# Performance work log

Hardware: AMD Instinct MI355X
Metric: run time of the kernel (lower is better)

Reference implementation:

```python
import jax, jax.numpy as jnp
import numpy as np

N = 100000   # nodes
E = 1600000  # edges
F_IN = 64    # n_features
H = 32       # hidden_size
OUT = 1      # output_size


def _lin(k, fan_in, fan_out):
    return (jax.random.normal(k, (fan_in, fan_out), jnp.float32) / np.sqrt(fan_in)).astype(jnp.float32)


def setup_inputs() -> dict:
    key = jax.random.key(0)
    ks = jax.random.split(key, 16)
    x = jax.random.normal(ks[0], (N, F_IN), jnp.float32)
    edge_index = jax.random.randint(ks[1], (2, E), 0, N, dtype=jnp.int64)
    # guarantee current_node (=0) has outgoing edges so the legal-move mask is non-empty
    edge_index = edge_index.at[0, :64].set(0)
    edge_attr = jax.random.uniform(ks[2], (E,), jnp.float32)
    return {
        "x": x, "edge_index": edge_index, "edge_attr": edge_attr, "current_node": 0,
        # conv_in: GraphConv(F_IN -> H)
        "Win_rel": _lin(ks[3], F_IN, H), "bin_rel": jnp.zeros((H,), jnp.float32), "Win_root": _lin(ks[4], F_IN, H),
        # conv_hidden: GraphConv(H -> H)
        "Wh_rel": _lin(ks[5], H, H), "bh_rel": jnp.zeros((H,), jnp.float32), "Wh_root": _lin(ks[6], H, H),
        # policy_conv: GraphConv(H -> OUT)
        "Wp_rel": _lin(ks[7], H, OUT), "bp_rel": jnp.zeros((OUT,), jnp.float32), "Wp_root": _lin(ks[8], H, OUT),
        # value_conv: GraphConv(H -> OUT)
        "Wv_rel": _lin(ks[9], H, OUT), "bv_rel": jnp.zeros((OUT,), jnp.float32), "Wv_root": _lin(ks[10], H, OUT),
    }


def _graph_conv(h, src, dst, ew, W_rel, b_rel, W_root):
    # PyG GraphConv: out_i = W_root h_i + W_rel * sum_{j->i} e_ji * h_j + b
    msg = h[src] * ew[:, None]                              # [E, d] gather + scale
    agg = jax.ops.segment_sum(msg, dst, num_segments=N)      # [N, d] scatter-add
    return agg @ W_rel + b_rel + h @ W_root


def reference(x, edge_index, edge_attr, current_node,
              Win_rel, bin_rel, Win_root,
              Wh_rel, bh_rel, Wh_root,
              Wp_rel, bp_rel, Wp_root,
              Wv_rel, bv_rel, Wv_root):
    src, dst = edge_index[0], edge_index[1]
    h = jax.nn.relu(_graph_conv(x, src, dst, edge_attr, Win_rel, bin_rel, Win_root))
    h = jax.nn.relu(_graph_conv(h, src, dst, edge_attr, Wh_rel, bh_rel, Wh_root))
    p = _graph_conv(h, src, dst, edge_attr, Wp_rel, bp_rel, Wp_root)  # [N, 1]
    v = _graph_conv(h, src, dst, edge_attr, Wv_rel, bv_rel, Wv_root)  # [N, 1]
    # illegal_moves_mask: 1 for nodes directly reachable from current_node
    hit = (src == current_node).astype(jnp.float32)
    mask = (jnp.zeros((N,), jnp.float32).at[dst].add(hit) > 0).astype(jnp.float32)
    p_m = mask * p.T                                   # [1, N]
    p_m = jnp.where(p_m == 0, -jnp.inf, p_m)
    p_soft = jax.nn.softmax(p_m, axis=1)
    v_m = mask * v.T                                   # [1, N]
    return p_soft.reshape(-1), v_m.reshape(-1)
```

## Files before the change

kernel.cpp:

```cpp
#include <hip/hip_runtime.h>
#include <hip/hip_fp16.h>
#include <cmath>

static constexpr int NN = 100000;
static constexpr int NE = 1600000;
static const size_t NW = (size_t)NN * 32;
static constexpr int SUB = 256;
static constexpr int NSUB = 391;
static constexpr int CH = 8192;
static constexpr int NCH = (NE + CH - 1) / CH;
static constexpr int BCAP = 5200;
static constexpr int CSRN = NSUB * BCAP;
static constexpr int MCAP = 4096;
static constexpr int NCAP = 8192;

__device__ __forceinline__ float ent_w(unsigned e)
{
    return __half2float(__ushort_as_half((unsigned short)(e >> 17)));
}
__device__ __forceinline__ int ent_s(unsigned e)
{
    int s = (int)(e & 0x1FFFF);
    return s < NN ? s : NN - 1;
}

__device__ __forceinline__ float4 pack8(const float* v)
{
    union { __half2 h2[4]; float4 f4; } u;
    u.h2[0] = __floats2half2_rn(v[0], v[1]);
    u.h2[1] = __floats2half2_rn(v[2], v[3]);
    u.h2[2] = __floats2half2_rn(v[4], v[5]);
    u.h2[3] = __floats2half2_rn(v[6], v[7]);
    return u.f4;
}

__device__ __forceinline__ int wave_incl_scan(int v, int lane)
{
    int s = v;
#pragma unroll
    for (int d = 1; d < 64; d <<= 1) {
        int o = __shfl_up(s, d, 64);
        if (lane >= d) s += o;
    }
    return s;
}

__global__ void __launch_bounds__(512) fused_build_mm1_k(
    const int* __restrict__ src, const int* __restrict__ dst,
    const float* __restrict__ ew, const int* __restrict__ curp,
    int* __restrict__ maskb, int* __restrict__ mcount, int* __restrict__ mlist,
    int* __restrict__ bcnt, unsigned* __restrict__ bx,
    unsigned char* __restrict__ bd,
    const float* __restrict__ x, const float* __restrict__ Wrel,
    const float* __restrict__ Wroot, const float* __restrict__ bin,
    __half* __restrict__ proj1, __half* __restrict__ root1)
{
    __shared__ union {
        struct {
            unsigned sBufX[CH];
            unsigned char sBufD[CH];
            int lhist[NSUB];
            int lpos[NSUB];
            int lstart[NSUB];
            int lbase[NSUB];
            int tscan[512];
        } s;
        struct {
            float sX[128 * 65];
            float sW[64 * 68];
        } m;
    } u;

    int t = threadIdx.x;
    int bid = blockIdx.x;

    if (bid < NCH) {
        for (int i = t; i < NSUB; i += 512) { u.s.lhist[i] = 0; u.s.lpos[i] = 0; }
        __syncthreads();
        int c0 = bid * CH;
        int cur = curp[0];
        unsigned rx[CH / 512];
        int rd[CH / 512];
#pragma unroll
        for (int it = 0; it < CH / 512; ++it) {
            int e = c0 + it * 512 + t;
            rd[it] = -1;
            if (e < NE) {
                int d = dst[e];
                int sv = src[e];
                if ((unsigned)d < (unsigned)NN) {
                    rd[it] = d;
                    unsigned bits = __half_as_ushort(__float2half(ew[e]));
                    rx[it] = ((unsigned)sv & 0x1FFFF) | (bits << 17);
                    atomicAdd(&u.s.lhist[d >> 8], 1);
                    if (sv == cur) {
                        if (atomicExch(maskb + d, 1) == 0) {
                            int idx = atomicAdd(mcount, 1);
                            if (idx < MCAP) mlist[idx] = d;
                        }
                    }
                }
            }
        }
        __syncthreads();
        {
            int v = (t < NSUB) ? u.s.lhist[t] : 0;
            int lane = t & 63, wv = t >> 6;
            int sI = wave_incl_scan(v, lane);
            if (lane == 63) u.s.tscan[wv] = sI;
            __syncthreads();
            if (t == 0) {
                int r = 0;
#pragma unroll
                for (int w2 = 0; w2 < 8; ++w2) {
                    int xw = u.s.tscan[w2];
                    u.s.tscan[8 + w2] = r;
                    r += xw;
                }
            }
            __syncthreads();
            if (t < NSUB) {
                u.s.lstart[t] = sI + u.s.tscan[8 + wv] - v;
                u.s.lbase[t] = (v > 0) ? atomicAdd(&bcnt[t], v) : 0;
            }
        }
        __syncthreads();
#pragma unroll
        for (int it = 0; it < CH / 512; ++it) {
            if (rd[it] >= 0) {
                int b = rd[it] >> 8;
                int p = atomicAdd(&u.s.lpos[b], 1);
                int pos = u.s.lstart[b] + p;
                u.s.sBufX[pos] = rx[it];
                u.s.sBufD[pos] = (unsigned char)(rd[it] & 255);
            }
        }
        __syncthreads();
        int grp = t >> 4, l16 = t & 15;
        for (int b = grp; b < NSUB; b += 32) {
            int s0 = u.s.lstart[b];
            int cb = u.s.lhist[b];
            int gb = u.s.lbase[b];
            size_t gb0 = (size_t)b * BCAP;
            for (int j = l16; j < cb; j += 16) {
                unsigned pos = (unsigned)(gb + j);
                if (pos < (unsigned)BCAP) {
                    bx[gb0 + pos] = u.s.sBufX[s0 + j];
                    bd[gb0 + pos] = u.s.sBufD[s0 + j];
                }
            }
        }
    } else {
        int mb = bid - NCH;
        for (int i = t; i < 64 * 32; i += 512) {
            int k = i >> 5, j = i & 31;
            u.m.sW[k * 68 + j] = Wrel[i];
            u.m.sW[k * 68 + 32 + j] = Wroot[i];
        }
        int base = mb * 128;
        for (int i = t; i < 2048; i += 512) {
            int node = i >> 4;
            int k = (i & 15) * 4;
            int n = base + node;
            if (n >= NN) n = NN - 1;
            float4 v4 = *(const float4*)(x + (size_t)n * 64 + k);
            float* p = u.m.sX + node * 65 + k;
            p[0] = v4.x; p[1] = v4.y; p[2] = v4.z; p[3] = v4.w;
        }
        __syncthreads();
        int cg = t & 7;
        int ng = t >> 3;
        int c0m = 8 * cg;
        float acc[2][8] = {};
        for (int k = 0; k < 64; ++k) {
            float xv0 = u.m.sX[(2 * ng + 0) * 65 + k];
            float xv1 = u.m.sX[(2 * ng + 1) * 65 + k];
            float4 w0 = *(const float4*)(u.m.sW + k * 68 + c0m);
            float4 w1 = *(const float4*)(u.m.sW + k * 68 + c0m + 4);
            const float* wp = (const float*)&w0;
#pragma unroll
            for (int j = 0; j < 4; ++j) {
                float w = wp[j];
                acc[0][j] = fmaf(xv0, w, acc[0][j]);
                acc[1][j] = fmaf(xv1, w, acc[1][j]);
            }
            const float* wq = (const float*)&w1;
#pragma unroll
            for (int j = 0; j < 4; ++j) {
                float w = wq[j];
                acc[0][4 + j] = fmaf(xv0, w, acc[0][4 + j]);
                acc[1][4 + j] = fmaf(xv1, w, acc[1][4 + j]);
            }
        }
#pragma unroll
        for (int r = 0; r < 2; ++r) {
            int n = base + 2 * ng + r;
            if (n >= NN) break;
            if (cg < 4) {
                *(float4*)(proj1 + (size_t)n * 32 + c0m) = pack8(acc[r]);
            } else {
                int c = c0m - 32;
                float vv[8];
#pragma unroll
                for (int j = 0; j < 8; ++j) vv[j] = acc[r][j] + bin[c + j];
                *(float4*)(root1 + (size_t)n * 32 + c) = pack8(vv);
            }
        }
    }
}

__global__ void __launch_bounds__(1024) sortagg1_k(
    const unsigned* __restrict__ bx, const unsigned char* __restrict__ bd,
    const int* __restrict__ bcnt, const int* __restrict__ maskb,
    int* __restrict__ needb, int* __restrict__ ncount,
    int* __restrict__ needlist,
    const __half* __restrict__ proj1, const __half* __restrict__ root1,
    unsigned* __restrict__ csr4, int* __restrict__ deg, int* __restrict__ off,
    __half* __restrict__ h1)
{
    __shared__ unsigned sX[BCAP];
    __shared__ unsigned char sD[BCAP];
    __shared__ unsigned sE[BCAP];
    __shared__ int lhist[SUB];
    __shared__ int lstart[SUB];
    __shared__ int lcur[SUB];
    __shared__ int tscan[16];
    int g = blockIdx.x, t = threadIdx.x;
    if (t < SUB) { lhist[t] = 0; lcur[t] = 0; }
    __syncthreads();
    int cnt = bcnt[g];
    if (cnt < 0) cnt = 0;
    if (cnt > BCAP) cnt = BCAP;
    size_t gbase = (size_t)g * BCAP;
    for (int i = t; i < cnt; i += 1024) {
        unsigned e = bx[gbase + i];
        unsigned char d = bd[gbase + i];
        sX[i] = e;
        sD[i] = d;
        atomicAdd(&lhist[d], 1);
    }
    __syncthreads();
    {
        int v = (t < SUB) ? lhist[t] : 0;
        int lane = t & 63, wv = t >> 6;
        int sI = wave_incl_scan(v, lane);
        if (t < SUB && lane == 63) tscan[wv] = sI;
        __syncthreads();
        if (t == 0) {
            int r = 0;
#pragma unroll
            for (int w2 = 0; w2 < 4; ++w2) {
                int xw = tscan[w2];
                tscan[8 + w2] = r;
                r += xw;
            }
        }
        __syncthreads();
        if (t < SUB) lstart[t] = sI + tscan[8 + wv] - v;
    }
    __syncthreads();
    for (int i = t; i < cnt; i += 1024) {
        int ld = (int)sD[i];
        int p = atomicAdd(&lcur[ld], 1);
        int pos = lstart[ld] + p;
        if ((unsigned)pos < (unsigned)BCAP) sE[pos] = sX[i];
    }
    __syncthreads();
    int base = g * BCAP;
    if (t < SUB) {
        int n = g * SUB + t;
        if (n < NN) {
            deg[n] = lhist[t];
            off[n] = base + lstart[t];
            if (maskb[n] != 0) {
                if (atomicExch(needb + n, 1) == 0) {
                    int ix = atomicAdd(ncount, 1);
                    if (ix < NCAP) needlist[ix] = n;
                }
                int s0 = lstart[t], dgn = lhist[t];
                for (int i2 = 0; i2 < dgn; ++i2) {
                    int s = ent_s(sE[s0 + i2]);
                    if (atomicExch(needb + s, 1) == 0) {
                        int ix = atomicAdd(ncount, 1);
                        if (ix < NCAP) needlist[ix] = s;
                    }
                }
            }
        }
    }
    for (int i = t; i < cnt; i += 1024) {
        unsigned pos = (unsigned)(base + i);
        if (pos < (unsigned)CSRN) csr4[pos] = sE[i];
    }
    int q = t & 3;
    int f0 = q * 8;
    int l = t >> 2;
    int n = g * SUB + l;
    if (n >= NN) return;
    int st = lstart[l];
    int dg = lhist[l];
    if (st < 0) st = 0;
    if (st > BCAP) st = BCAP;
    if (dg < 0) dg = 0;
    if (dg > BCAP - st) dg = BCAP - st;
    float acc[8] = {0.f, 0.f, 0.f, 0.f, 0.f, 0.f, 0.f, 0.f};
    int i = 0;
    for (; i + 1 < dg; i += 2) {
        unsigned e0 = sE[st + i];
        unsigned e1 = sE[st + i + 1];
        float w0 = ent_w(e0), w1 = ent_w(e1);
        float4 r0 = *(const float4*)(proj1 + (size_t)ent_s(e0) * 32 + f0);
        float4 r1 = *(const float4*)(proj1 + (size_t)ent_s(e1) * 32 + f0);
        const __half2* h0 = (const __half2*)&r0;
        const __half2* h1p = (const __half2*)&r1;
#pragma unroll
        for (int u = 0; u < 4; ++u) {
            float2 a = __half22float2(h0[u]);
            float2 b = __half22float2(h1p[u]);
            acc[2 * u] = fmaf(w0, a.x, acc[2 * u]);
            acc[2 * u + 1] = fmaf(w0, a.y, acc[2 * u + 1]);
            acc[2 * u] = fmaf(w1, b.x, acc[2 * u]);
            acc[2 * u + 1] = fmaf(w1, b.y, acc[2 * u + 1]);
        }
    }
    if (i < dg) {
        unsigned e0 = sE[st + i];
        float w0 = ent_w(e0);
        float4 r0 = *(const float4*)(proj1 + (size_t)ent_s(e0) * 32 + f0);
        const __half2* h0 = (const __half2*)&r0;
#pragma unroll
        for (int u = 0; u < 4; ++u) {
            float2 a = __half22float2(h0[u]);
            acc[2 * u] = fmaf(w0, a.x, acc[2 * u]);
            acc[2 * u + 1] = fmaf(w0, a.y, acc[2 * u + 1]);
        }
    }
    float4 rr = *(const float4*)(root1 + (size_t)n * 32 + f0);
    const __half2* rp = (const __half2*)&rr;
    float h[8];
#pragma unroll
    for (int u = 0; u < 4; ++u) {
        float2 f2 = __half22float2(rp[u]);
        h[2 * u] = fmaxf(acc[2 * u] + f2.x, 0.f);
        h[2 * u + 1] = fmaxf(acc[2 * u + 1] + f2.y, 0.f);
    }
    *(float4*)(h1 + (size_t)n * 32 + f0) = pack8(h);
}

__global__ void __launch_bounds__(256) mm2_k(
    const __half* __restrict__ h1, const float* __restrict__ Wrel,
    const float* __restrict__ Wroot, const float* __restrict__ bh,
    __half* __restrict__ proj2, __half* __restrict__ root2)
{
    __shared__ float sX[128 * 33];
    __shared__ float sW[32 * 68];
    int t = threadIdx.x;
    for (int i = t; i < 32 * 32; i += 256) {
        int k = i >> 5, j = i & 31;
        sW[k * 68 + j] = Wrel[i];
        sW[k * 68 + 32 + j] = Wroot[i];
    }
    int base = blockIdx.x * 128;
    for (int i = t; i < 512; i += 256) {
        int node = i >> 2;
        int hs = (i & 3) * 8;
        int n = base + node;
        if (n >= NN) n = NN - 1;
        float4 v = *(const float4*)(h1 + (size_t)n * 32 + hs);
        const __half2* hp = (const __half2*)&v;
        float* p = sX + node * 33 + hs;
#pragma unroll
        for (int u = 0; u < 4; ++u) {
            float2 f2 = __half22float2(hp[u]);
            p[2 * u] = f2.x;
            p[2 * u + 1] = f2.y;
        }
    }
    __syncthreads();
    int cg = t & 7;
    int ng = t >> 3;
    int c0 = 8 * cg;
    float acc[4][8] = {};
    for (int k = 0; k < 32; ++k) {
        float xv0 = sX[(4 * ng + 0) * 33 + k];
        float xv1 = sX[(4 * ng + 1) * 33 + k];
        float xv2 = sX[(4 * ng + 2) * 33 + k];
        float xv3 = sX[(4 * ng + 3) * 33 + k];
        float4 w0 = *(const float4*)(sW + k * 68 + c0);
        float4 w1 = *(const float4*)(sW + k * 68 + c0 + 4);
        const float* wp = (const float*)&w0;
#pragma unroll
        for (int j = 0; j < 4; ++j) {
            float w = wp[j];
            acc[0][j] = fmaf(xv0, w, acc[0][j]);
            acc[1][j] = fmaf(xv1, w, acc[1][j]);
            acc[2][j] = fmaf(xv2, w, acc[2][j]);
            acc[3][j] = fmaf(xv3, w, acc[3][j]);
        }
        const float* wq = (const float*)&w1;
#pragma unroll
        for (int j = 0; j < 4; ++j) {
            float w = wq[j];
            acc[0][4 + j] = fmaf(xv0, w, acc[0][4 + j]);
            acc[1][4 + j] = fmaf(xv1, w, acc[1][4 + j]);
            acc[2][4 + j] = fmaf(xv2, w, acc[2][4 + j]);
            acc[3][4 + j] = fmaf(xv3, w, acc[3][4 + j]);
        }
    }
#pragma unroll
    for (int r = 0; r < 4; ++r) {
        int n = base + 4 * ng + r;
        if (n >= NN) break;
        if (cg < 4) {
            *(float4*)(proj2 + (size_t)n * 32 + c0) = pack8(acc[r]);
        } else {
            int c = c0 - 32;
            float v[8];
#pragma unroll
            for (int j = 0; j < 8; ++j) v[j] = acc[r][j] + bh[c + j];
            *(float4*)(root2 + (size_t)n * 32 + c) = pack8(v);
        }
    }
}

__global__ void __launch_bounds__(256) need_gather_k(
    const __half* __restrict__ proj2, const __half* __restrict__ root2,
    const float* __restrict__ Wp_rel, const float* __restrict__ Wp_root,
    const float* __restrict__ bp, const float* __restrict__ Wv_rel,
    const float* __restrict__ Wv_root, const float* __restrict__ bv,
    const unsigned* __restrict__ csr4, const int* __restrict__ off,
    const int* __restrict__ deg, const int* __restrict__ needlist,
    const int* __restrict__ ncount, float2* __restrict__ pv,
    float* __restrict__ pbase, float* __restrict__ vbase)
{
    __shared__ float sHead[4 * 32];
    if (threadIdx.x < 32) {
        sHead[threadIdx.x] = Wp_rel[threadIdx.x];
        sHead[32 + threadIdx.x] = Wp_root[threadIdx.x];
        sHead[64 + threadIdx.x] = Wv_rel[threadIdx.x];
        sHead[96 + threadIdx.x] = Wv_root[threadIdx.x];
    }
    __syncthreads();
    int t = threadIdx.x;
    int q = t & 3;
    int f0 = q * 8;
    int m = ncount[0];
    if (m > NCAP) m = NCAP;
    int idx = blockIdx.x * 64 + (t >> 2);
    if (idx >= m) return;
    int n = needlist[idx];
    if ((unsigned)n >= (unsigned)NN) n = 0;
    int st = off[n];
    int dg = deg[n];
    if (st < 0) st = 0;
    if (st > CSRN) st = CSRN;
    if (dg < 0) dg = 0;
    if (dg > CSRN - st) dg = CSRN - st;
    float acc[8] = {0.f, 0.f, 0.f, 0.f, 0.f, 0.f, 0.f, 0.f};
    int i = 0;
    for (; i + 3 < dg; i += 4) {
        unsigned e0 = csr4[st + i];
        unsigned e1 = csr4[st + i + 1];
        unsigned e2 = csr4[st + i + 2];
        unsigned e3 = csr4[st + i + 3];
        float4 r0 = *(const float4*)(proj2 + (size_t)ent_s(e0) * 32 + f0);
        float4 r1 = *(const float4*)(proj2 + (size_t)ent_s(e1) * 32 + f0);
        float4 r2 = *(const float4*)(proj2 + (size_t)ent_s(e2) * 32 + f0);
        float4 r3 = *(const float4*)(proj2 + (size_t)ent_s(e3) * 32 + f0);
        float w0 = ent_w(e0), w1 = ent_w(e1), w2 = ent_w(e2), w3 = ent_w(e3);
        const __half2* h0 = (const __half2*)&r0;
        const __half2* h1p = (const __half2*)&r1;
        const __half2* h2p = (const __half2*)&r2;
        const __half2* h3p = (const __half2*)&r3;
#pragma unroll
        for (int u = 0; u < 4; ++u) {
            float2 a = __half22float2(h0[u]);
            float2 b = __half22float2(h1p[u]);
            float2 c = __half22float2(h2p[u]);
            float2 d = __half22float2(h3p[u]);
            acc[2 * u]     = fmaf(w0, a.x, acc[2 * u]);
            acc[2 * u + 1] = fmaf(w0, a.y, acc[2 * u + 1]);
            acc[2 * u]     = fmaf(w1, b.x, acc[2 * u]);
            acc[2 * u + 1] = fmaf(w1, b.y, acc[2 * u + 1]);
            acc[2 * u]     = fmaf(w2, c.x, acc[2 * u]);
            acc[2 * u + 1] = fmaf(w2, c.y, acc[2 * u + 1]);
            acc[2 * u]     = fmaf(w3, d.x, acc[2 * u]);
            acc[2 * u + 1] = fmaf(w3, d.y, acc[2 * u + 1]);
        }
    }
    for (; i < dg; ++i) {
        unsigned e0 = csr4[st + i];
        float w0 = ent_w(e0);
        float4 r0 = *(const float4*)(proj2 + (size_t)ent_s(e0) * 32 + f0);
        const __half2* h0 = (const __half2*)&r0;
#pragma unroll
        for (int u = 0; u < 4; ++u) {
            float2 a = __half22float2(h0[u]);
            acc[2 * u] = fmaf(w0, a.x, acc[2 * u]);
            acc[2 * u + 1] = fmaf(w0, a.y, acc[2 * u + 1]);
        }
    }
    float4 rr = *(const float4*)(root2 + (size_t)n * 32 + f0);
    const __half2* rp = (const __half2*)&rr;
    float h[8];
#pragma unroll
    for (int u = 0; u < 4; ++u) {
        float2 f2 = __half22float2(rp[u]);
        h[2 * u] = fmaxf(acc[2 * u] + f2.x, 0.f);
        h[2 * u + 1] = fmaxf(acc[2 * u + 1] + f2.y, 0.f);
    }
    float prv = 0.f, pov = 0.f, vrv = 0.f, vov = 0.f;
#pragma unroll
    for (int j = 0; j < 8; ++j) {
        prv = fmaf(h[j], sHead[f0 + j], prv);
        pov = fmaf(h[j], sHead[32 + f0 + j], pov);
        vrv = fmaf(h[j], sHead[64 + f0 + j], vrv);
        vov = fmaf(h[j], sHead[96 + f0 + j], vov);
    }
#pragma unroll
    for (int mm = 1; mm <= 2; mm <<= 1) {
        prv += __shfl_xor(prv, mm, 64);
        pov += __shfl_xor(pov, mm, 64);
        vrv += __shfl_xor(vrv, mm, 64);
        vov += __shfl_xor(vov, mm, 64);
    }
    if (q == 0) {
        pv[n] = make_float2(prv, vrv);
        pbase[n] = pov + bp[0];
        vbase[n] = vov + bv[0];
    }
}

__global__ void __launch_bounds__(256) masked_softmax_k(
    const int* __restrict__ mlist, const int* __restrict__ mcount,
    const unsigned* __restrict__ csr4, const int* __restrict__ off,
    const int* __restrict__ deg, const float2* __restrict__ pv,
    const float* __restrict__ pbase, const float* __restrict__ vbase,
    float* __restrict__ out_p, float* __restrict__ out_v)
{
    __shared__ float sPm[MCAP];
    __shared__ float sV[MCAP];
    __shared__ int sN[MCAP];
    __shared__ float sMx, sSum;
    __shared__ float sred[4];
    int m = mcount[0];
    if (m > MCAP) m = MCAP;
    if (m < 0) m = 0;
    int lane4 = threadIdx.x & 3;
    for (int idx = threadIdx.x >> 2; idx < m; idx += 64) {
        int n = mlist[idx];
        if ((unsigned)n >= (unsigned)NN) n = 0;
        int st = off[n];
        int dg = deg[n];
        if (st < 0) st = 0;
        if (st > CSRN) st = CSRN;
        if (dg < 0) dg = 0;
        if (dg > CSRN - st) dg = CSRN - st;
        float pa = 0.f, va = 0.f;
        for (int i = lane4; i < dg; i += 4) {
            unsigned ent = csr4[st + i];
            int s = ent_s(ent);
            float w = ent_w(ent);
            float2 tv = pv[s];
            pa = fmaf(tv.x, w, pa);
            va = fmaf(tv.y, w, va);
        }
        pa += __shfl_xor(pa, 1, 64);
        pa += __shfl_xor(pa, 2, 64);
        va += __shfl_xor(va, 1, 64);
        va += __shfl_xor(va, 2, 64);
        if (lane4 == 0) {
            sN[idx] = n;
            float p = pa + pbase[n];
            sPm[idx] = (p == 0.f) ? -INFINITY : p;
            sV[idx] = va + vbase[n];
        }
    }
    __syncthreads();
    float mx = -INFINITY;
    for (int i = threadIdx.x; i < m; i += 256) mx = fmaxf(mx, sPm[i]);
#pragma unroll
    for (int k = 32; k; k >>= 1) mx = fmaxf(mx, __shfl_xor(mx, k, 64));
    if ((threadIdx.x & 63) == 0) sred[threadIdx.x >> 6] = mx;
    __syncthreads();
    if (threadIdx.x == 0)
        sMx = fmaxf(fmaxf(sred[0], sred[1]), fmaxf(sred[2], sred[3]));
    __syncthreads();
    float sum = 0.f;
    for (int i = threadIdx.x; i < m; i += 256) {
        float x = sPm[i];
        sum += (x == -INFINITY) ? 0.f : expf(x - sMx);
    }
#pragma unroll
    for (int k = 32; k; k >>= 1) sum += __shfl_xor(sum, k, 64);
    if ((threadIdx.x & 63) == 0) sred[threadIdx.x >> 6] = sum;
    __syncthreads();
    if (threadIdx.x == 0) sSum = sred[0] + sred[1] + sred[2] + sred[3];
    __syncthreads();
    for (int idx = threadIdx.x; idx < m; idx += 256) {
        int n = sN[idx];
        float x = sPm[idx];
        out_p[n] = (x == -INFINITY) ? 0.f : expf(x - sMx) / sSum;
        out_v[n] = sV[idx];
    }
}

extern "C" void kernel_launch(void* const* d_in, const int* in_sizes, int n_in,
                              void* d_out, int out_size, void* d_ws,
                              size_t ws_size, hipStream_t stream)
{
    const float* x        = (const float*)d_in[0];
    const int*   ei       = (const int*)d_in[1];
    const float* ew       = (const float*)d_in[2];
    const int*   cur      = (const int*)d_in[3];
    const float* Win_rel  = (const float*)d_in[4];
    const float* bin_rel  = (const float*)d_in[5];
    const float* Win_root = (const float*)d_in[6];
    const float* Wh_rel   = (const float*)d_in[7];
    const float* bh_rel   = (const float*)d_in[8];
    const float* Wh_root  = (const float*)d_in[9];
    const float* Wp_rel   = (const float*)d_in[10];
    const float* bp       = (const float*)d_in[11];
    const float* Wp_root  = (const float*)d_in[12];
    const float* Wv_rel   = (const float*)d_in[13];
    const float* bv       = (const float*)d_in[14];
    const float* Wv_root  = (const float*)d_in[15];

    const int* srcA = ei;
    const int* dstA = ei + NE;

    char* w8 = (char*)d_ws;
    unsigned* csr4 = (unsigned*)w8;
    int* deg    = (int*)(csr4 + CSRN);
    int* off    = deg + NN;
    int* maskb  = off + NN;
    int* mcount = maskb + NN;
    int* bcnt   = mcount + 8;
    int* needb  = bcnt + 400;
    int* ncnt   = needb + NN;
    int* mlist  = ncnt + 8;
    int* needlist = mlist + MCAP;
    __half* proj1 = (__half*)(needlist + NCAP);
    __half* root1 = proj1 + NW;
    __half* h1    = root1 + NW;
    __half* proj2 = h1 + NW;
    __half* root2 = proj2 + NW;
    float2* pv    = (float2*)(root2 + NW);
    float* pbase  = (float*)(pv + NN);
    float* vbase  = pbase + NN;
    unsigned* bucket_x = (unsigned*)(vbase + NN);
    unsigned char* bucket_d = (unsigned char*)(bucket_x + CSRN);

    float* out_p = (float*)d_out;
    float* out_v = out_p + NN;

    const int NB_MM    = (NN + 127) / 128;
    const int NB_FUSED = NCH + NB_MM;
    const int NB_NEED  = NCAP / 64;

    hipMemsetAsync(maskb, 0, ((size_t)2 * NN + 416) * sizeof(int), stream);
    hipMemsetAsync(d_out, 0, 2 * (size_t)NN * sizeof(float), stream);

    fused_build_mm1_k<<<NB_FUSED, 512, 0, stream>>>(
        srcA, dstA, ew, cur, maskb, mcount, mlist, bcnt, bucket_x, bucket_d,
        x, Win_rel, Win_root, bin_rel, proj1, root1);
    sortagg1_k<<<NSUB, 1024, 0, stream>>>(bucket_x, bucket_d, bcnt, maskb,
                                          needb, ncnt, needlist,
                                          proj1, root1, csr4, deg, off, h1);
    mm2_k<<<NB_MM, 256, 0, stream>>>(h1, Wh_rel, Wh_root, bh_rel, proj2, root2);
    need_gather_k<<<NB_NEED, 256, 0, stream>>>(
        proj2, root2, Wp_rel, Wp_root, bp, Wv_rel, Wv_root, bv,
        csr4, off, deg, needlist, ncnt, pv, pbase, vbase);
    masked_softmax_k<<<1, 256, 0, stream>>>(mlist, mcount, csr4, off, deg, pv,
                                            pbase, vbase, out_p, out_v);
}
```

Measured before the change: 214.9 us.

## Restrict layer-1 aggregation to the two-hop dependency set of masked nodes

```diff
diff --git a/kernel.cpp b/kernel.cpp
--- a/kernel.cpp
+++ b/kernel.cpp
@@ -13,6 +13,7 @@
 static constexpr int CSRN = NSUB * BCAP;
 static constexpr int MCAP = 4096;
 static constexpr int NCAP = 8192;
+static constexpr int NCAP2 = 65536;
 
 __device__ __forceinline__ float ent_w(unsigned e)
 {
@@ -209,14 +210,12 @@
     }
 }
 
-__global__ void __launch_bounds__(1024) sortagg1_k(
+__global__ void __launch_bounds__(1024) sortmark_k(
     const unsigned* __restrict__ bx, const unsigned char* __restrict__ bd,
     const int* __restrict__ bcnt, const int* __restrict__ maskb,
     int* __restrict__ needb, int* __restrict__ ncount,
     int* __restrict__ needlist,
-    const __half* __restrict__ proj1, const __half* __restrict__ root1,
-    unsigned* __restrict__ csr4, int* __restrict__ deg, int* __restrict__ off,
-    __half* __restrict__ h1)
+    unsigned* __restrict__ csr4, int* __restrict__ deg, int* __restrict__ off)
 {
     __shared__ unsigned sX[BCAP];
     __shared__ unsigned char sD[BCAP];
@@ -292,39 +291,97 @@
         unsigned pos = (unsigned)(base + i);
         if (pos < (unsigned)CSRN) csr4[pos] = sE[i];
     }
+}
+
+__global__ void __launch_bounds__(256) need2_build_k(
+    const int* __restrict__ needlist, const int* __restrict__ ncount,
+    const unsigned* __restrict__ csr4, const int* __restrict__ off,
+    const int* __restrict__ deg, int* __restrict__ need2b,
+    int* __restrict__ n2cnt, int* __restrict__ need2list)
+{
+    int m = ncount[0];
+    if (m > NCAP) m = NCAP;
+    if (m < 0) m = 0;
+    int gid = blockIdx.x * 256 + threadIdx.x;
+    int stride = gridDim.x * 256;
+    for (int idx = gid; idx < m; idx += stride) {
+        int n = needlist[idx];
+        if ((unsigned)n >= (unsigned)NN) n = 0;
+        if (atomicExch(need2b + n, 1) == 0) {
+            int ix = atomicAdd(n2cnt, 1);
+            if (ix < NCAP2) need2list[ix] = n;
+        }
+        int st = off[n];
+        int dg = deg[n];
+        if (st < 0) st = 0;
+        if (st > CSRN) st = CSRN;
+        if (dg < 0) dg = 0;
+        if (dg > CSRN - st) dg = CSRN - st;
+        for (int i = 0; i < dg; ++i) {
+            int s = ent_s(csr4[st + i]);
+            if (atomicExch(need2b + s, 1) == 0) {
+                int ix = atomicAdd(n2cnt, 1);
+                if (ix < NCAP2) need2list[ix] = s;
+            }
+        }
+    }
+}
+
+__global__ void __launch_bounds__(256) agg1_need2_k(
+    const __half* __restrict__ proj1, const __half* __restrict__ root1,
+    const unsigned* __restrict__ csr4, const int* __restrict__ off,
+    const int* __restrict__ deg, const int* __restrict__ need2list,
+    const int* __restrict__ n2cnt, __half* __restrict__ h1)
+{
+    int t = threadIdx.x;
     int q = t & 3;
     int f0 = q * 8;
-    int l = t >> 2;
-    int n = g * SUB + l;
-    if (n >= NN) return;
-    int st = lstart[l];
-    int dg = lhist[l];
+    int m = n2cnt[0];
+    if (m > NCAP2) m = NCAP2;
+    int idx = blockIdx.x * 64 + (t >> 2);
+    if (idx >= m) return;
+    int n = need2list[idx];
+    if ((unsigned)n >= (unsigned)NN) n = 0;
+    int st = off[n];
+    int dg = deg[n];
     if (st < 0) st = 0;
-    if (st > BCAP) st = BCAP;
+    if (st > CSRN) st = CSRN;
     if (dg < 0) dg = 0;
-    if (dg > BCAP - st) dg = BCAP - st;
+    if (dg > CSRN - st) dg = CSRN - st;
     float acc[8] = {0.f, 0.f, 0.f, 0.f, 0.f, 0.f, 0.f, 0.f};
     int i = 0;
-    for (; i + 1 < dg; i += 2) {
-        unsigned e0 = sE[st + i];
-        unsigned e1 = sE[st + i + 1];
-        float w0 = ent_w(e0), w1 = ent_w(e1);
+    for (; i + 3 < dg; i += 4) {
+        unsigned e0 = csr4[st + i];
+        unsigned e1 = csr4[st + i + 1];
+        unsigned e2 = csr4[st + i + 2];
+        unsigned e3 = csr4[st + i + 3];
         float4 r0 = *(const float4*)(proj1 + (size_t)ent_s(e0) * 32 + f0);
         float4 r1 = *(const float4*)(proj1 + (size_t)ent_s(e1) * 32 + f0);
+        float4 r2 = *(const float4*)(proj1 + (size_t)ent_s(e2) * 32 + f0);
+        float4 r3 = *(const float4*)(proj1 + (size_t)ent_s(e3) * 32 + f0);
+        float w0 = ent_w(e0), w1 = ent_w(e1), w2 = ent_w(e2), w3 = ent_w(e3);
         const __half2* h0 = (const __half2*)&r0;
         const __half2* h1p = (const __half2*)&r1;
+        const __half2* h2p = (const __half2*)&r2;
+        const __half2* h3p = (const __half2*)&r3;
 #pragma unroll
         for (int u = 0; u < 4; ++u) {
             float2 a = __half22float2(h0[u]);
             float2 b = __half22float2(h1p[u]);
-            acc[2 * u] = fmaf(w0, a.x, acc[2 * u]);
+            float2 c = __half22float2(h2p[u]);
+            float2 d = __half22float2(h3p[u]);
+            acc[2 * u]     = fmaf(w0, a.x, acc[2 * u]);
             acc[2 * u + 1] = fmaf(w0, a.y, acc[2 * u + 1]);
-            acc[2 * u] = fmaf(w1, b.x, acc[2 * u]);
+            acc[2 * u]     = fmaf(w1, b.x, acc[2 * u]);
             acc[2 * u + 1] = fmaf(w1, b.y, acc[2 * u + 1]);
-        }
-    }
-    if (i < dg) {
-        unsigned e0 = sE[st + i];
+            acc[2 * u]     = fmaf(w2, c.x, acc[2 * u]);
+            acc[2 * u + 1] = fmaf(w2, c.y, acc[2 * u + 1]);
+            acc[2 * u]     = fmaf(w3, d.x, acc[2 * u]);
+            acc[2 * u + 1] = fmaf(w3, d.y, acc[2 * u + 1]);
+        }
+    }
+    for (; i < dg; ++i) {
+        unsigned e0 = csr4[st + i];
         float w0 = ent_w(e0);
         float4 r0 = *(const float4*)(proj1 + (size_t)ent_s(e0) * 32 + f0);
         const __half2* h0 = (const __half2*)&r0;
@@ -638,9 +695,12 @@
     int* bcnt   = mcount + 8;
     int* needb  = bcnt + 400;
     int* ncnt   = needb + NN;
-    int* mlist  = ncnt + 8;
+    int* need2b = ncnt + 8;
+    int* n2cnt  = need2b + NN;
+    int* mlist  = n2cnt + 8;
     int* needlist = mlist + MCAP;
-    __half* proj1 = (__half*)(needlist + NCAP);
+    int* need2list = needlist + NCAP;
+    __half* proj1 = (__half*)(need2list + NCAP2);
     __half* root1 = proj1 + NW;
     __half* h1    = root1 + NW;
     __half* proj2 = h1 + NW;
@@ -657,16 +717,21 @@
     const int NB_MM    = (NN + 127) / 128;
     const int NB_FUSED = NCH + NB_MM;
     const int NB_NEED  = NCAP / 64;
-
-    hipMemsetAsync(maskb, 0, ((size_t)2 * NN + 416) * sizeof(int), stream);
+    const int NB_NEED2 = NCAP2 / 64;
+
+    hipMemsetAsync(maskb, 0, ((size_t)3 * NN + 424) * sizeof(int), stream);
     hipMemsetAsync(d_out, 0, 2 * (size_t)NN * sizeof(float), stream);
 
     fused_build_mm1_k<<<NB_FUSED, 512, 0, stream>>>(
         srcA, dstA, ew, cur, maskb, mcount, mlist, bcnt, bucket_x, bucket_d,
         x, Win_rel, Win_root, bin_rel, proj1, root1);
-    sortagg1_k<<<NSUB, 1024, 0, stream>>>(bucket_x, bucket_d, bcnt, maskb,
+    sortmark_k<<<NSUB, 1024, 0, stream>>>(bucket_x, bucket_d, bcnt, maskb,
                                           needb, ncnt, needlist,
-                                          proj1, root1, csr4, deg, off, h1);
+                                          csr4, deg, off);
+    need2_build_k<<<16, 256, 0, stream>>>(needlist, ncnt, csr4, off, deg,
+                                          need2b, n2cnt, need2list);
+    agg1_need2_k<<<NB_NEED2, 256, 0, stream>>>(proj1, root1, csr4, off, deg,
+                                               need2list, n2cnt, h1);
     mm2_k<<<NB_MM, 256, 0, stream>>>(h1, Wh_rel, Wh_root, bh_rel, proj2, root2);
     need_gather_k<<<NB_NEED, 256, 0, stream>>>(
         proj2, root2, Wp_rel, Wp_root, bp, Wv_rel, Wv_root, bv,
```

Result: slower. 250.5 us (+16.6%).
